# Kernel tuning notes

Hardware: AMD Instinct MI355X
Metric: run time of the kernel (lower is better)

The kernel has to match this reference:

```python
import jax, jax.numpy as jnp
import numpy as np


def setup_inputs() -> dict:
    key = jax.random.key(0)
    k1, k2, k3, k4 = jax.random.split(key, 4)
    B, S, E, H = 8, 2048, 1024, 64
    x = jax.random.normal(k1, (B, S, E), dtype=jnp.float32)
    # nn.Linear(E, H, bias=False) weight is (H, E); we store transposed (E, H)
    scale = 1.0 / np.sqrt(E)
    Wk = jax.random.normal(k2, (E, H), dtype=jnp.float32) * scale
    Wq = jax.random.normal(k3, (E, H), dtype=jnp.float32) * scale
    Wv = jax.random.normal(k4, (E, H), dtype=jnp.float32) * scale
    return {"x": x, "Wk": Wk, "Wq": Wq, "Wv": Wv}


def reference(x, Wk, Wq, Wv):
    # x: (B, S, E); projections: (B, S, H)
    k = x @ Wk
    q = x @ Wq
    v = x @ Wv
    H = k.shape[-1]
    # scores: (B, S, S) with 1/sqrt(H) scaling as in the torch code
    scores = jnp.einsum("bqh,bkh->bqk", q, k) * (H ** -0.5)
    S = x.shape[1]
    causal = jnp.triu(jnp.full((S, S), -jnp.inf, dtype=scores.dtype), k=1)
    wei = jax.nn.softmax(scores + causal, axis=-1)
    # dropout p=0.0 -> identity
    return jnp.einsum("bqk,bkh->bqh", wei, v)
```

## Files before the change

kernel.cpp:

```cpp
#include <hip/hip_runtime.h>
#include <hip/hip_bf16.h>

typedef unsigned short ushort_t;
typedef __attribute__((ext_vector_type(8))) short short8;
typedef __attribute__((ext_vector_type(4))) float f32x4;

__device__ __forceinline__ float bf2f(ushort_t u) {
    unsigned int x = ((unsigned int)u) << 16;
    float f; __builtin_memcpy(&f, &x, 4); return f;
}
__device__ __forceinline__ ushort_t f2bf(float f) {
    unsigned int x; __builtin_memcpy(&x, &f, 4);
    x += 0x7fff + ((x >> 16) & 1);
    return (ushort_t)(x >> 16);
}

constexpr int E  = 1024;
constexpr int Hd = 64;
constexpr int S  = 2048;
constexpr int ROWS = 8 * 2048;
constexpr int NTOT = 192;
constexpr int LST  = 88;

__global__ __launch_bounds__(256)
void prep_wt(const float* __restrict__ Wk, const float* __restrict__ Wq,
             const float* __restrict__ Wv, ushort_t* __restrict__ WT)
{
    int idx = blockIdx.x * 256 + threadIdx.x;
    int n = idx >> 10;
    int kk = idx & 1023;
    const float* W = (n < 64) ? Wq : ((n < 128) ? Wk : Wv);
    int h = n & 63;
    WT[idx] = f2bf(W[kk * Hd + h]);
}

__global__ __launch_bounds__(256, 1)
void proj_v6(const float* __restrict__ x, const ushort_t* __restrict__ WT,
             ushort_t* __restrict__ qo, ushort_t* __restrict__ ko,
             ushort_t* __restrict__ vTo)
{
    __shared__ alignas(16) ushort_t XS[64][LST];

    const int t    = threadIdx.x;
    const int w    = t >> 6;
    const int lane = t & 63;
    const int m    = lane & 15;
    const int g    = lane >> 4;
    const int rb   = blockIdx.x * 64;

    f32x4 acc[3][4];
    #pragma unroll
    for (int j = 0; j < 3; ++j)
        #pragma unroll
        for (int mt = 0; mt < 4; ++mt) acc[j][mt] = (f32x4){0.f, 0.f, 0.f, 0.f};

    const float* xptr = x + (size_t)(rb + (t >> 2)) * E + (t & 3) * 16;
    const ushort_t* wq = WT + (size_t)(w * 16 + m) * E       + g * 8;
    const ushort_t* wk = WT + (size_t)(64 + w * 16 + m) * E  + g * 8;
    const ushort_t* wv = WT + (size_t)(128 + w * 16 + m) * E + g * 8;

    float4 xp[4];
    short8 bp[3][2], bc[3][2];

    #pragma unroll
    for (int j = 0; j < 4; ++j) xp[j] = *(const float4*)(xptr + j * 4);
    #pragma unroll
    for (int kt = 0; kt < 2; ++kt) {
        bp[0][kt] = *(const short8*)(wq + kt * 32);
        bp[1][kt] = *(const short8*)(wk + kt * 32);
        bp[2][kt] = *(const short8*)(wv + kt * 32);
    }

    #pragma unroll 1
    for (int c = 0; c < 16; ++c) {
        {
            short8 s0, s1;
            s0[0]=(short)f2bf(xp[0].x); s0[1]=(short)f2bf(xp[0].y);
            s0[2]=(short)f2bf(xp[0].z); s0[3]=(short)f2bf(xp[0].w);
            s0[4]=(short)f2bf(xp[1].x); s0[5]=(short)f2bf(xp[1].y);
            s0[6]=(short)f2bf(xp[1].z); s0[7]=(short)f2bf(xp[1].w);
            s1[0]=(short)f2bf(xp[2].x); s1[1]=(short)f2bf(xp[2].y);
            s1[2]=(short)f2bf(xp[2].z); s1[3]=(short)f2bf(xp[2].w);
            s1[4]=(short)f2bf(xp[3].x); s1[5]=(short)f2bf(xp[3].y);
            s1[6]=(short)f2bf(xp[3].z); s1[7]=(short)f2bf(xp[3].w);
            *(short8*)&XS[t >> 2][(t & 3) * 16]     = s0;
            *(short8*)&XS[t >> 2][(t & 3) * 16 + 8] = s1;
        }
        #pragma unroll
        for (int j = 0; j < 3; ++j) { bc[j][0] = bp[j][0]; bc[j][1] = bp[j][1]; }
        __syncthreads();

        if (c < 15) {
            const int k0 = (c + 1) * 64;
            #pragma unroll
            for (int j = 0; j < 4; ++j) xp[j] = *(const float4*)(xptr + k0 + j * 4);
            #pragma unroll
            for (int kt = 0; kt < 2; ++kt) {
                bp[0][kt] = *(const short8*)(wq + k0 + kt * 32);
                bp[1][kt] = *(const short8*)(wk + k0 + kt * 32);
                bp[2][kt] = *(const short8*)(wv + k0 + kt * 32);
            }
        }

        #pragma unroll
        for (int kt = 0; kt < 2; ++kt) {
            short8 a[4];
            #pragma unroll
            for (int mt = 0; mt < 4; ++mt)
                a[mt] = *(const short8*)&XS[mt * 16 + m][kt * 32 + g * 8];
            #pragma unroll
            for (int mt = 0; mt < 4; ++mt) {
                acc[0][mt] = __builtin_amdgcn_mfma_f32_16x16x32_bf16(a[mt], bc[0][kt], acc[0][mt], 0, 0, 0);
                acc[1][mt] = __builtin_amdgcn_mfma_f32_16x16x32_bf16(a[mt], bc[1][kt], acc[1][mt], 0, 0, 0);
                acc[2][mt] = __builtin_amdgcn_mfma_f32_16x16x32_bf16(a[mt], bc[2][kt], acc[2][mt], 0, 0, 0);
            }
        }
        __syncthreads();
    }

    const int col   = w * 16 + m;
    const int batch = rb >> 11;
    const int seq0  = rb & (S - 1);
    #pragma unroll
    for (int mt = 0; mt < 4; ++mt) {
        const int orow = rb + mt * 16 + g * 4;
        #pragma unroll
        for (int r = 0; r < 4; ++r) {
            qo[(size_t)(orow + r) * Hd + col] = f2bf(acc[0][mt][r] * 0.125f);
            ko[(size_t)(orow + r) * Hd + col] = f2bf(acc[1][mt][r]);
            vTo[(size_t)batch * Hd * S + (size_t)col * S + seq0 + mt * 16 + g * 4 + r]
                = f2bf(acc[2][mt][r]);
        }
    }
}

__global__ __launch_bounds__(256)
void attn_part(const ushort_t* __restrict__ q, const ushort_t* __restrict__ k,
               const ushort_t* __restrict__ vT, float* __restrict__ mp,
               float* __restrict__ lp, ushort_t* __restrict__ op)
{
    const int bi     = blockIdx.x;
    const int parity = bi & 1;
    const int pr     = bi >> 1;
    const int tile   = 31 - (pr >> 3);
    const int batch  = pr & 7;
    const int qs0    = tile * 64;
    const int sidx   = (batch * 32 + tile) * 2 + parity;

    const ushort_t* kb  = k  + (size_t)batch * S * Hd;
    const ushort_t* vTb = vT + (size_t)batch * Hd * S;

    const int t    = threadIdx.x;
    const int w    = t >> 6;
    const int lane = t & 63;
    const int m    = lane & 15;
    const int g    = lane >> 4;

    __shared__ alignas(16) ushort_t KS [64][LST];
    __shared__ alignas(16) ushort_t VTS[64][LST];
    __shared__ alignas(16) ushort_t PL[4][16][LST];

    const ushort_t* qrow = q + (size_t)(batch * S + qs0 + w * 16 + m) * Hd;
    short8 qf0 = *(const short8*)(qrow + g * 8);
    short8 qf1 = *(const short8*)(qrow + 32 + g * 8);

    f32x4 o[4];
    #pragma unroll
    for (int j = 0; j < 4; ++j) o[j] = (f32x4){0.f, 0.f, 0.f, 0.f};
    float mrun[4] = {-INFINITY, -INFINITY, -INFINITY, -INFINITY};
    float lrun[4] = {0.f, 0.f, 0.f, 0.f};

    const int r1 = t >> 3, c16 = (t & 7) * 8;
    uint4 pk0, pk1, pv0, pv1;

    int c = parity;
    if (c <= tile) {
        const int key0 = c * 64;
        const ushort_t* kt_base = kb + (size_t)key0 * Hd;
        pk0 = *(const uint4*)(kt_base + t * 8);
        pk1 = *(const uint4*)(kt_base + (t + 256) * 8);
        pv0 = *(const uint4*)(vTb + (size_t)r1 * S + key0 + c16);
        pv1 = *(const uint4*)(vTb + (size_t)(r1 + 32) * S + key0 + c16);
    }

    for (; c <= tile; c += 2) {
        *(uint4*)&KS [t >> 3][c16]        = pk0;
        *(uint4*)&KS [(t >> 3) + 32][c16] = pk1;
        *(uint4*)&VTS[r1][c16]            = pv0;
        *(uint4*)&VTS[r1 + 32][c16]       = pv1;
        __syncthreads();

        if (c + 2 <= tile) {
            const int key0n = (c + 2) * 64;
            const ushort_t* kt_base = kb + (size_t)key0n * Hd;
            pk0 = *(const uint4*)(kt_base + t * 8);
            pk1 = *(const uint4*)(kt_base + (t + 256) * 8);
            pv0 = *(const uint4*)(vTb + (size_t)r1 * S + key0n + c16);
            pv1 = *(const uint4*)(vTb + (size_t)(r1 + 32) * S + key0n + c16);
        }

        f32x4 sacc[4];
        #pragma unroll
        for (int j = 0; j < 4; ++j) sacc[j] = (f32x4){0.f, 0.f, 0.f, 0.f};
        #pragma unroll
        for (int nt = 0; nt < 4; ++nt) {
            short8 b0 = *(const short8*)&KS[nt * 16 + m][g * 8];
            short8 b1 = *(const short8*)&KS[nt * 16 + m][32 + g * 8];
            sacc[nt] = __builtin_amdgcn_mfma_f32_16x16x32_bf16(qf0, b0, sacc[nt], 0, 0, 0);
            sacc[nt] = __builtin_amdgcn_mfma_f32_16x16x32_bf16(qf1, b1, sacc[nt], 0, 0, 0);
        }

        if (c == tile) {
            const int rowl = w * 16 + g * 4;
            #pragma unroll
            for (int nt = 0; nt < 4; ++nt) {
                const int keyl = nt * 16 + m;
                #pragma unroll
                for (int r = 0; r < 4; ++r)
                    if (keyl > rowl + r) sacc[nt][r] = -INFINITY;
            }
        }

        float msafe[4], alpha[4];
        #pragma unroll
        for (int r = 0; r < 4; ++r) {
            float tm = fmaxf(fmaxf(sacc[0][r], sacc[1][r]),
                             fmaxf(sacc[2][r], sacc[3][r]));
            #pragma unroll
            for (int d = 1; d < 16; d <<= 1) tm = fmaxf(tm, __shfl_xor(tm, d, 64));
            float mn = fmaxf(mrun[r], tm);
            msafe[r] = (mn == -INFINITY) ? 0.f : mn;
            alpha[r] = __expf(mrun[r] - msafe[r]);
            mrun[r]  = mn;
        }
        #pragma unroll
        for (int nt = 0; nt < 4; ++nt)
            #pragma unroll
            for (int r = 0; r < 4; ++r)
                sacc[nt][r] = __expf(sacc[nt][r] - msafe[r]);
        #pragma unroll
        for (int r = 0; r < 4; ++r) {
            float ts = sacc[0][r] + sacc[1][r] + sacc[2][r] + sacc[3][r];
            #pragma unroll
            for (int d = 1; d < 16; d <<= 1) ts += __shfl_xor(ts, d, 64);
            lrun[r] = lrun[r] * alpha[r] + ts;
        }
        #pragma unroll
        for (int nt = 0; nt < 4; ++nt)
            #pragma unroll
            for (int r = 0; r < 4; ++r)
                o[nt][r] *= alpha[r];

        #pragma unroll
        for (int nt = 0; nt < 4; ++nt)
            #pragma unroll
            for (int r = 0; r < 4; ++r)
                PL[w][g * 4 + r][nt * 16 + m] = f2bf(sacc[nt][r]);

        short8 pa0 = *(const short8*)&PL[w][m][g * 8];
        short8 pa1 = *(const short8*)&PL[w][m][32 + g * 8];

        #pragma unroll
        for (int nt = 0; nt < 4; ++nt) {
            short8 vb0 = *(const short8*)&VTS[nt * 16 + m][g * 8];
            short8 vb1 = *(const short8*)&VTS[nt * 16 + m][32 + g * 8];
            o[nt] = __builtin_amdgcn_mfma_f32_16x16x32_bf16(pa0, vb0, o[nt], 0, 0, 0);
            o[nt] = __builtin_amdgcn_mfma_f32_16x16x32_bf16(pa1, vb1, o[nt], 0, 0, 0);
        }
        __syncthreads();
    }

    if (m == 0) {
        #pragma unroll
        for (int r = 0; r < 4; ++r) {
            mp[sidx * 64 + w * 16 + g * 4 + r] = mrun[r];
            lp[sidx * 64 + w * 16 + g * 4 + r] = lrun[r];
        }
    }
    #pragma unroll
    for (int nt = 0; nt < 4; ++nt)
        #pragma unroll
        for (int r = 0; r < 4; ++r)
            op[(size_t)sidx * 4096 + (w * 16 + g * 4 + r) * 64 + nt * 16 + m]
                = f2bf(o[nt][r]);
}

__global__ __launch_bounds__(256)
void attn_merge(const float* __restrict__ mp, const float* __restrict__ lp,
                const ushort_t* __restrict__ op, float* __restrict__ out)
{
    const int bq    = blockIdx.x;
    const int batch = bq >> 5;
    const int tile  = bq & 31;
    const int s0    = (batch * 32 + tile) * 2;

    const int t   = threadIdx.x;
    const int row = t >> 2;
    const int c16 = (t & 3) * 16;

    float m0 = mp[s0 * 64 + row],       m1 = mp[(s0 + 1) * 64 + row];
    float l0 = lp[s0 * 64 + row],       l1 = lp[(s0 + 1) * 64 + row];
    float M  = fmaxf(m0, m1);
    float w0 = __expf(m0 - M), w1 = __expf(m1 - M);
    float inv = 1.f / (w0 * l0 + w1 * l1);

    short8 a0 = *(const short8*)(op + (size_t)s0 * 4096 + row * 64 + c16);
    short8 a1 = *(const short8*)(op + (size_t)s0 * 4096 + row * 64 + c16 + 8);
    short8 b0 = *(const short8*)(op + (size_t)(s0 + 1) * 4096 + row * 64 + c16);
    short8 b1 = *(const short8*)(op + (size_t)(s0 + 1) * 4096 + row * 64 + c16 + 8);

    float* dst = out + (size_t)(batch * S + tile * 64 + row) * Hd + c16;
    #pragma unroll
    for (int j = 0; j < 8; ++j)
        dst[j]     = (w0 * bf2f((ushort_t)a0[j]) + w1 * bf2f((ushort_t)b0[j])) * inv;
    #pragma unroll
    for (int j = 0; j < 8; ++j)
        dst[j + 8] = (w0 * bf2f((ushort_t)a1[j]) + w1 * bf2f((ushort_t)b1[j])) * inv;
}

extern "C" void kernel_launch(void* const* d_in, const int* in_sizes, int n_in,
                              void* d_out, int out_size, void* d_ws, size_t ws_size,
                              hipStream_t stream) {
    const float* x  = (const float*)d_in[0];
    const float* Wk = (const float*)d_in[1];
    const float* Wq = (const float*)d_in[2];
    const float* Wv = (const float*)d_in[3];
    float* out = (float*)d_out;

    ushort_t* qws  = (ushort_t*)d_ws;
    ushort_t* kws  = qws + (size_t)ROWS * Hd;
    ushort_t* vTws = kws + (size_t)ROWS * Hd;
    ushort_t* WT   = vTws + (size_t)ROWS * Hd;
    float*    mpp  = (float*)(WT + (size_t)NTOT * E);
    float*    lpp  = mpp + 512 * 64;
    ushort_t* opp  = (ushort_t*)(lpp + 512 * 64);

    prep_wt<<<(NTOT * E) / 256, 256, 0, stream>>>(Wk, Wq, Wv, WT);
    proj_v6<<<ROWS / 64, 256, 0, stream>>>(x, WT, qws, kws, vTws);
    attn_part<<<512, 256, 0, stream>>>(qws, kws, vTws, mpp, lpp, opp);
    attn_merge<<<256, 256, 0, stream>>>(mpp, lpp, opp, out);
}
```

Baseline: 150.1 us.

## Halve projection row tile and split attention keys four ways

The projection kernel now handles 32 rows per block instead of 64, doubling the grid to 512 blocks. It also computes V with swapped MFMA operands so the transposed V store writes contiguous sequence positions. The attention split-K goes from two to four key-interleaved partitions (1024 blocks), and the merge kernel combines four partials. The aim is more parallelism and better load balance across CUs for the causal attention, at the cost of more partial-output traffic and reloading the weights twice as often in the projection.

Result: faster. 142.1 us (-5.3%).

```diff
diff --git a/kernel.cpp b/kernel.cpp
--- a/kernel.cpp
+++ b/kernel.cpp
@@ -34,86 +34,83 @@
     WT[idx] = f2bf(W[kk * Hd + h]);
 }
 
-__global__ __launch_bounds__(256, 1)
-void proj_v6(const float* __restrict__ x, const ushort_t* __restrict__ WT,
+__global__ __launch_bounds__(256)
+void proj_v7(const float* __restrict__ x, const ushort_t* __restrict__ WT,
              ushort_t* __restrict__ qo, ushort_t* __restrict__ ko,
              ushort_t* __restrict__ vTo)
 {
-    __shared__ alignas(16) ushort_t XS[64][LST];
+    __shared__ alignas(16) ushort_t XS[32][LST];
 
     const int t    = threadIdx.x;
     const int w    = t >> 6;
     const int lane = t & 63;
     const int m    = lane & 15;
     const int g    = lane >> 4;
-    const int rb   = blockIdx.x * 64;
-
-    f32x4 acc[3][4];
-    #pragma unroll
-    for (int j = 0; j < 3; ++j)
-        #pragma unroll
-        for (int mt = 0; mt < 4; ++mt) acc[j][mt] = (f32x4){0.f, 0.f, 0.f, 0.f};
-
-    const float* xptr = x + (size_t)(rb + (t >> 2)) * E + (t & 3) * 16;
-    const ushort_t* wq = WT + (size_t)(w * 16 + m) * E       + g * 8;
-    const ushort_t* wk = WT + (size_t)(64 + w * 16 + m) * E  + g * 8;
-    const ushort_t* wv = WT + (size_t)(128 + w * 16 + m) * E + g * 8;
-
-    float4 xp[4];
-    short8 bp[3][2], bc[3][2];
-
-    #pragma unroll
-    for (int j = 0; j < 4; ++j) xp[j] = *(const float4*)(xptr + j * 4);
+    const int rb   = blockIdx.x * 32;
+
+    f32x4 accq[2], acck[2], accv[2];
+    #pragma unroll
+    for (int j = 0; j < 2; ++j) {
+        accq[j] = (f32x4){0.f, 0.f, 0.f, 0.f};
+        acck[j] = (f32x4){0.f, 0.f, 0.f, 0.f};
+        accv[j] = (f32x4){0.f, 0.f, 0.f, 0.f};
+    }
+
+    const float* xptr = x + (size_t)(rb + (t >> 3)) * E + (t & 7) * 8;
+    const ushort_t* wqp = WT + (size_t)(w * 16 + m) * E + g * 8;
+    const ushort_t* wkp = wqp + (size_t)64 * E;
+    const ushort_t* wvp = wqp + (size_t)128 * E;
+
+    float4 xp0, xp1;
+    short8 pbq[2], pbk[2], pbv[2], cbq[2], cbk[2], cbv[2];
+
+    xp0 = *(const float4*)xptr;
+    xp1 = *(const float4*)(xptr + 4);
     #pragma unroll
     for (int kt = 0; kt < 2; ++kt) {
-        bp[0][kt] = *(const short8*)(wq + kt * 32);
-        bp[1][kt] = *(const short8*)(wk + kt * 32);
-        bp[2][kt] = *(const short8*)(wv + kt * 32);
+        pbq[kt] = *(const short8*)(wqp + kt * 32);
+        pbk[kt] = *(const short8*)(wkp + kt * 32);
+        pbv[kt] = *(const short8*)(wvp + kt * 32);
     }
 
     #pragma unroll 1
     for (int c = 0; c < 16; ++c) {
         {
-            short8 s0, s1;
-            s0[0]=(short)f2bf(xp[0].x); s0[1]=(short)f2bf(xp[0].y);
-            s0[2]=(short)f2bf(xp[0].z); s0[3]=(short)f2bf(xp[0].w);
-            s0[4]=(short)f2bf(xp[1].x); s0[5]=(short)f2bf(xp[1].y);
-            s0[6]=(short)f2bf(xp[1].z); s0[7]=(short)f2bf(xp[1].w);
-            s1[0]=(short)f2bf(xp[2].x); s1[1]=(short)f2bf(xp[2].y);
-            s1[2]=(short)f2bf(xp[2].z); s1[3]=(short)f2bf(xp[2].w);
-            s1[4]=(short)f2bf(xp[3].x); s1[5]=(short)f2bf(xp[3].y);
-            s1[6]=(short)f2bf(xp[3].z); s1[7]=(short)f2bf(xp[3].w);
-            *(short8*)&XS[t >> 2][(t & 3) * 16]     = s0;
-            *(short8*)&XS[t >> 2][(t & 3) * 16 + 8] = s1;
-        }
-        #pragma unroll
-        for (int j = 0; j < 3; ++j) { bc[j][0] = bp[j][0]; bc[j][1] = bp[j][1]; }
+            short8 s;
+            s[0]=(short)f2bf(xp0.x); s[1]=(short)f2bf(xp0.y);
+            s[2]=(short)f2bf(xp0.z); s[3]=(short)f2bf(xp0.w);
+            s[4]=(short)f2bf(xp1.x); s[5]=(short)f2bf(xp1.y);
+            s[6]=(short)f2bf(xp1.z); s[7]=(short)f2bf(xp1.w);
+            *(short8*)&XS[t >> 3][(t & 7) * 8] = s;
+        }
+        #pragma unroll
+        for (int kt = 0; kt < 2; ++kt) {
+            cbq[kt] = pbq[kt]; cbk[kt] = pbk[kt]; cbv[kt] = pbv[kt];
+        }
         __syncthreads();
 
         if (c < 15) {
             const int k0 = (c + 1) * 64;
-            #pragma unroll
-            for (int j = 0; j < 4; ++j) xp[j] = *(const float4*)(xptr + k0 + j * 4);
+            xp0 = *(const float4*)(xptr + k0);
+            xp1 = *(const float4*)(xptr + k0 + 4);
             #pragma unroll
             for (int kt = 0; kt < 2; ++kt) {
-                bp[0][kt] = *(const short8*)(wq + k0 + kt * 32);
-                bp[1][kt] = *(const short8*)(wk + k0 + kt * 32);
-                bp[2][kt] = *(const short8*)(wv + k0 + kt * 32);
+                pbq[kt] = *(const short8*)(wqp + k0 + kt * 32);
+                pbk[kt] = *(const short8*)(wkp + k0 + kt * 32);
+                pbv[kt] = *(const short8*)(wvp + k0 + kt * 32);
             }
         }
 
         #pragma unroll
         for (int kt = 0; kt < 2; ++kt) {
-            short8 a[4];
-            #pragma unroll
-            for (int mt = 0; mt < 4; ++mt)
-                a[mt] = *(const short8*)&XS[mt * 16 + m][kt * 32 + g * 8];
-            #pragma unroll
-            for (int mt = 0; mt < 4; ++mt) {
-                acc[0][mt] = __builtin_amdgcn_mfma_f32_16x16x32_bf16(a[mt], bc[0][kt], acc[0][mt], 0, 0, 0);
-                acc[1][mt] = __builtin_amdgcn_mfma_f32_16x16x32_bf16(a[mt], bc[1][kt], acc[1][mt], 0, 0, 0);
-                acc[2][mt] = __builtin_amdgcn_mfma_f32_16x16x32_bf16(a[mt], bc[2][kt], acc[2][mt], 0, 0, 0);
-            }
+            short8 a0 = *(const short8*)&XS[m][kt * 32 + g * 8];
+            short8 a1 = *(const short8*)&XS[16 + m][kt * 32 + g * 8];
+            accq[0] = __builtin_amdgcn_mfma_f32_16x16x32_bf16(a0, cbq[kt], accq[0], 0, 0, 0);
+            accq[1] = __builtin_amdgcn_mfma_f32_16x16x32_bf16(a1, cbq[kt], accq[1], 0, 0, 0);
+            acck[0] = __builtin_amdgcn_mfma_f32_16x16x32_bf16(a0, cbk[kt], acck[0], 0, 0, 0);
+            acck[1] = __builtin_amdgcn_mfma_f32_16x16x32_bf16(a1, cbk[kt], acck[1], 0, 0, 0);
+            accv[0] = __builtin_amdgcn_mfma_f32_16x16x32_bf16(cbv[kt], a0, accv[0], 0, 0, 0);
+            accv[1] = __builtin_amdgcn_mfma_f32_16x16x32_bf16(cbv[kt], a1, accv[1], 0, 0, 0);
         }
         __syncthreads();
     }
@@ -122,16 +119,22 @@
     const int batch = rb >> 11;
     const int seq0  = rb & (S - 1);
     #pragma unroll
-    for (int mt = 0; mt < 4; ++mt) {
+    for (int mt = 0; mt < 2; ++mt) {
         const int orow = rb + mt * 16 + g * 4;
         #pragma unroll
         for (int r = 0; r < 4; ++r) {
-            qo[(size_t)(orow + r) * Hd + col] = f2bf(acc[0][mt][r] * 0.125f);
-            ko[(size_t)(orow + r) * Hd + col] = f2bf(acc[1][mt][r]);
-            vTo[(size_t)batch * Hd * S + (size_t)col * S + seq0 + mt * 16 + g * 4 + r]
-                = f2bf(acc[2][mt][r]);
-        }
-    }
+            qo[(size_t)(orow + r) * Hd + col] = f2bf(accq[mt][r] * 0.125f);
+            ko[(size_t)(orow + r) * Hd + col] = f2bf(acck[mt][r]);
+        }
+    }
+    #pragma unroll
+    for (int ns = 0; ns < 2; ++ns)
+        #pragma unroll
+        for (int r = 0; r < 4; ++r) {
+            const int h = w * 16 + g * 4 + r;
+            vTo[(size_t)batch * Hd * S + (size_t)h * S + seq0 + ns * 16 + m]
+                = f2bf(accv[ns][r]);
+        }
 }
 
 __global__ __launch_bounds__(256)
@@ -140,12 +143,12 @@
                float* __restrict__ lp, ushort_t* __restrict__ op)
 {
     const int bi     = blockIdx.x;
-    const int parity = bi & 1;
-    const int pr     = bi >> 1;
+    const int parity = bi & 3;
+    const int pr     = bi >> 2;
+    const int batch  = pr & 7;
     const int tile   = 31 - (pr >> 3);
-    const int batch  = pr & 7;
     const int qs0    = tile * 64;
-    const int sidx   = (batch * 32 + tile) * 2 + parity;
+    const int sidx   = (batch * 32 + tile) * 4 + parity;
 
     const ushort_t* kb  = k  + (size_t)batch * S * Hd;
     const ushort_t* vTb = vT + (size_t)batch * Hd * S;
@@ -183,15 +186,15 @@
         pv1 = *(const uint4*)(vTb + (size_t)(r1 + 32) * S + key0 + c16);
     }
 
-    for (; c <= tile; c += 2) {
-        *(uint4*)&KS [t >> 3][c16]        = pk0;
-        *(uint4*)&KS [(t >> 3) + 32][c16] = pk1;
-        *(uint4*)&VTS[r1][c16]            = pv0;
-        *(uint4*)&VTS[r1 + 32][c16]       = pv1;
+    for (; c <= tile; c += 4) {
+        *(uint4*)&KS [r1][c16]       = pk0;
+        *(uint4*)&KS [r1 + 32][c16]  = pk1;
+        *(uint4*)&VTS[r1][c16]       = pv0;
+        *(uint4*)&VTS[r1 + 32][c16]  = pv1;
         __syncthreads();
 
-        if (c + 2 <= tile) {
-            const int key0n = (c + 2) * 64;
+        if (c + 4 <= tile) {
+            const int key0n = (c + 4) * 64;
             const ushort_t* kt_base = kb + (size_t)key0n * Hd;
             pk0 = *(const uint4*)(kt_base + t * 8);
             pk1 = *(const uint4*)(kt_base + (t + 256) * 8);
@@ -292,30 +295,41 @@
     const int bq    = blockIdx.x;
     const int batch = bq >> 5;
     const int tile  = bq & 31;
-    const int s0    = (batch * 32 + tile) * 2;
+    const int s0    = (batch * 32 + tile) * 4;
 
     const int t   = threadIdx.x;
     const int row = t >> 2;
     const int c16 = (t & 3) * 16;
 
-    float m0 = mp[s0 * 64 + row],       m1 = mp[(s0 + 1) * 64 + row];
-    float l0 = lp[s0 * 64 + row],       l1 = lp[(s0 + 1) * 64 + row];
-    float M  = fmaxf(m0, m1);
-    float w0 = __expf(m0 - M), w1 = __expf(m1 - M);
-    float inv = 1.f / (w0 * l0 + w1 * l1);
-
-    short8 a0 = *(const short8*)(op + (size_t)s0 * 4096 + row * 64 + c16);
-    short8 a1 = *(const short8*)(op + (size_t)s0 * 4096 + row * 64 + c16 + 8);
-    short8 b0 = *(const short8*)(op + (size_t)(s0 + 1) * 4096 + row * 64 + c16);
-    short8 b1 = *(const short8*)(op + (size_t)(s0 + 1) * 4096 + row * 64 + c16 + 8);
-
+    float mv[4], lv[4];
+    float M = -INFINITY;
+    #pragma unroll
+    for (int p = 0; p < 4; ++p) {
+        mv[p] = mp[(s0 + p) * 64 + row];
+        lv[p] = lp[(s0 + p) * 64 + row];
+        M = fmaxf(M, mv[p]);
+    }
+    float wgt[4], l = 0.f;
+    #pragma unroll
+    for (int p = 0; p < 4; ++p) { wgt[p] = __expf(mv[p] - M); l += wgt[p] * lv[p]; }
+    const float inv = 1.f / l;
+
+    float acc[16];
+    #pragma unroll
+    for (int j = 0; j < 16; ++j) acc[j] = 0.f;
+    #pragma unroll
+    for (int p = 0; p < 4; ++p) {
+        short8 a0 = *(const short8*)(op + (size_t)(s0 + p) * 4096 + row * 64 + c16);
+        short8 a1 = *(const short8*)(op + (size_t)(s0 + p) * 4096 + row * 64 + c16 + 8);
+        #pragma unroll
+        for (int j = 0; j < 8; ++j) {
+            acc[j]     += wgt[p] * bf2f((ushort_t)a0[j]);
+            acc[j + 8] += wgt[p] * bf2f((ushort_t)a1[j]);
+        }
+    }
     float* dst = out + (size_t)(batch * S + tile * 64 + row) * Hd + c16;
     #pragma unroll
-    for (int j = 0; j < 8; ++j)
-        dst[j]     = (w0 * bf2f((ushort_t)a0[j]) + w1 * bf2f((ushort_t)b0[j])) * inv;
-    #pragma unroll
-    for (int j = 0; j < 8; ++j)
-        dst[j + 8] = (w0 * bf2f((ushort_t)a1[j]) + w1 * bf2f((ushort_t)b1[j])) * inv;
+    for (int j = 0; j < 16; ++j) dst[j] = acc[j] * inv;
 }
 
 extern "C" void kernel_launch(void* const* d_in, const int* in_sizes, int n_in,
@@ -332,11 +346,11 @@
     ushort_t* vTws = kws + (size_t)ROWS * Hd;
     ushort_t* WT   = vTws + (size_t)ROWS * Hd;
     float*    mpp  = (float*)(WT + (size_t)NTOT * E);
-    float*    lpp  = mpp + 512 * 64;
-    ushort_t* opp  = (ushort_t*)(lpp + 512 * 64);
+    float*    lpp  = mpp + 1024 * 64;
+    ushort_t* opp  = (ushort_t*)(lpp + 1024 * 64);
 
     prep_wt<<<(NTOT * E) / 256, 256, 0, stream>>>(Wk, Wq, Wv, WT);
-    proj_v6<<<ROWS / 64, 256, 0, stream>>>(x, WT, qws, kws, vTws);
-    attn_part<<<512, 256, 0, stream>>>(qws, kws, vTws, mpp, lpp, opp);
+    proj_v7<<<ROWS / 32, 256, 0, stream>>>(x, WT, qws, kws, vTws);
+    attn_part<<<1024, 256, 0, stream>>>(qws, kws, vTws, mpp, lpp, opp);
     attn_merge<<<256, 256, 0, stream>>>(mpp, lpp, opp, out);
 }
```
